# Kernel tuning notes

Measured on AMD Instinct MI355X. Metric: run time of the kernel, lower is better.

Reference implementation:

```python
import jax, jax.numpy as jnp
import numpy as np

# ---- fixed architecture hyperparameters (match init_kwargs) ----
B, S = 4, 1024
L, H, DM, DF = 4, 8, 512, 2048
DH = DM // H          # 64 head dim (= 2*R after gated SPE filter)
NS = 5                # num_sines
R = 32                # num_realizations
M = 2 * DH            # favor_feature_dims = 128 (split as +/- of 64 projections)
LN_EPS = 1e-5
ATT_EPS = 1e-6


def layernorm(x, g, b):
    mu = x.mean(-1, keepdims=True)
    var = ((x - mu) ** 2).mean(-1, keepdims=True)
    return (x - mu) * jax.lax.rsqrt(var + LN_EPS) * g + b


def sine_spe(freqs, offsets, gains, noise, seq_len):
    """SineSPE positional code. freqs/offsets/gains: (H,DH,NS); noise: (H,DH,2NS,R).
    Returns qbar, kbar of shape (S,H,DH,R)."""
    pos = jnp.arange(seq_len, dtype=freqs.dtype)
    f = jax.nn.sigmoid(freqs)[:, :, None, :] / 2.0                       # (H,DH,1,NS)
    ph_q = 2.0 * jnp.pi * f * pos[None, None, :, None] + offsets[:, :, None, :]
    ph_k = 2.0 * jnp.pi * f * pos[None, None, :, None]
    om_q = jnp.stack([jnp.cos(ph_q), jnp.sin(ph_q)], -1).reshape(H, DH, seq_len, 2 * NS)
    om_k = jnp.stack([jnp.cos(ph_k), jnp.sin(ph_k)], -1).reshape(H, DH, seq_len, 2 * NS)
    g = jax.nn.softplus(gains)
    g = jnp.stack([g, g], -1).reshape(H, DH, 2 * NS)                      # upsample gains
    z = noise * g[..., None] / jnp.sqrt(jnp.asarray(2.0 * NS, freqs.dtype))
    qbar = jnp.einsum('hdsk,hdkr->shdr', om_q, z)
    kbar = jnp.einsum('hdsk,hdkr->shdr', om_k, z)
    scale = (R * DH) ** 0.25
    return qbar / scale, kbar / scale


def spe_filter(q, k, qbar, kbar, gate, gnoise):
    """Gated SPE filter. q,k: (B,S,H,DH); qbar/kbar: (S,H,DH,R); gate: (H,DH); gnoise: (H,DH,R).
    Returns qhat, khat of shape (B,S,H,2R)."""
    g = jax.nn.sigmoid(gate)[..., None]                                   # (H,DH,1)
    gn = gnoise / (DH * R) ** 0.25
    seq_len = qbar.shape[0]
    bias = jnp.broadcast_to(jnp.sqrt(g) * gn, (seq_len, H, DH, R))
    qb = jnp.concatenate([jnp.sqrt(1.0 - g) * qbar, bias], -1)            # (S,H,DH,2R)
    kb = jnp.concatenate([jnp.sqrt(1.0 - g) * kbar, bias], -1)
    qhat = jnp.einsum('bshd,shdr->bshr', q, qb)
    khat = jnp.einsum('bshd,shdr->bshr', k, kb)
    return qhat, khat


def favor(x, omega):
    """FAVOR+ softmax feature map. x: (B,S,H,DH); omega: (DH, M//2) -> (B,S,H,M)."""
    x = x * (DH ** -0.25)                                                 # sqrt(softmax_temp), temp=1/sqrt(DH)
    half_norm = 0.5 * jnp.sum(x * x, -1, keepdims=True)
    u = jnp.einsum('bshe,em->bshm', x, omega)
    phi = jnp.concatenate([jnp.exp(u - half_norm), jnp.exp(-u - half_norm)], -1)
    return phi / jnp.sqrt(jnp.asarray(M, x.dtype))


def causal_linear_attention(Q, K, V):
    """Causal linear (kernelized) attention via lax.scan. Q,K: (B,S,H,M); V: (B,S,H,DH)."""
    Bv = Q.shape[0]

    def step(carry, qkv):
        Skv, sk = carry
        q, k, v = qkv                                                     # (B,H,M),(B,H,M),(B,H,DH)
        Skv = Skv + jnp.einsum('bhm,bhd->bhmd', k, v)
        sk = sk + k
        num = jnp.einsum('bhm,bhmd->bhd', q, Skv)
        den = jnp.einsum('bhm,bhm->bh', q, sk) + ATT_EPS
        return (Skv, sk), num / den[..., None]

    init = (jnp.zeros((Bv, H, M, DH), Q.dtype), jnp.zeros((Bv, H, M), Q.dtype))
    xs = tuple(jnp.moveaxis(t, 1, 0) for t in (Q, K, V))
    _, out = jax.lax.scan(step, init, xs)
    return jnp.moveaxis(out, 0, 1)                                        # (B,S,H,DH)


def setup_inputs() -> dict:
    key = jax.random.key(0)
    ks = jax.random.split(key, 14)

    def rn(k, shape, scale=1.0):
        return jax.random.normal(k, shape, dtype=jnp.float32) * scale

    return {
        'x': rn(ks[0], (B, S, DM)),
        'Wq': rn(ks[1], (L, DM, DM), 0.02), 'bq': jnp.zeros((L, DM), jnp.float32),
        'Wk': rn(ks[2], (L, DM, DM), 0.02), 'bk': jnp.zeros((L, DM), jnp.float32),
        'Wv': rn(ks[3], (L, DM, DM), 0.02), 'bv': jnp.zeros((L, DM), jnp.float32),
        'Wo': rn(ks[4], (L, DM, DM), 0.02), 'bo': jnp.zeros((L, DM), jnp.float32),
        'W1': rn(ks[5], (L, DM, DF), 0.02), 'b1': jnp.zeros((L, DF), jnp.float32),
        'W2': rn(ks[6], (L, DF, DM), 0.02), 'b2': jnp.zeros((L, DM), jnp.float32),
        'ln1_g': jnp.ones((L, DM), jnp.float32), 'ln1_b': jnp.zeros((L, DM), jnp.float32),
        'ln2_g': jnp.ones((L, DM), jnp.float32), 'ln2_b': jnp.zeros((L, DM), jnp.float32),
        'spe_freqs': rn(ks[7], (L, H, DH, NS)),
        'spe_offsets': rn(ks[8], (L, H, DH, NS)),
        'spe_gains': rn(ks[9], (L, H, DH, NS)),
        'spe_noise': rn(ks[10], (L, H, DH, 2 * NS, R)),
        'gate': rn(ks[11], (L, H, DH)),
        'gate_noise': rn(ks[12], (L, H, DH, R)),
        'favor_omega': rn(ks[13], (L, DH, M // 2)),
    }


def reference(x, Wq, bq, Wk, bk, Wv, bv, Wo, bo, W1, b1, W2, b2,
              ln1_g, ln1_b, ln2_g, ln2_b,
              spe_freqs, spe_offsets, spe_gains, spe_noise, gate, gate_noise, favor_omega):
    Bv, Sv, _ = x.shape
    out = x
    for l in range(L):
        qbar, kbar = sine_spe(spe_freqs[l], spe_offsets[l], spe_gains[l], spe_noise[l], Sv)
        q = (out @ Wq[l] + bq[l]).reshape(Bv, Sv, H, DH)
        k = (out @ Wk[l] + bk[l]).reshape(Bv, Sv, H, DH)
        v = (out @ Wv[l] + bv[l]).reshape(Bv, Sv, H, DH)
        qh, kh = spe_filter(q, k, qbar, kbar, gate[l], gate_noise[l])
        Qf = favor(qh, favor_omega[l])
        Kf = favor(kh, favor_omega[l])
        att = causal_linear_attention(Qf, Kf, v).reshape(Bv, Sv, DM)
        att = att @ Wo[l] + bo[l]
        h = layernorm(out + att, ln1_g[l], ln1_b[l])
        y = jax.nn.relu(h @ W1[l] + b1[l]) @ W2[l] + b2[l]
        out = layernorm(h + y, ln2_g[l], ln2_b[l])
    return out
```

## Files before the change

### kernel.cpp

```cpp
#include <hip/hip_runtime.h>
#include <math.h>

#define BB 4
#define SS 1024
#define LL 4
#define HH 8
#define DM 512
#define DF 2048
#define DH 64
#define NS 5
#define RR 32
#define MM 128
#define NC 16
#define CHK 64
#define QKV_N 1536

#define INV_SQRT10   0.316227766016838f
#define INV_SCALE    0.148650889375340f
#define TEMP_SCALE   0.353553390593274f
#define INV_SQRT_M   0.088388347648318f
#define TWO_PI       6.283185307179586f

typedef __attribute__((ext_vector_type(8))) short bf16x8;
typedef __attribute__((ext_vector_type(4))) float f32x4;

__device__ __forceinline__ unsigned short f2bf(float f) {
  union { float f; unsigned int u; } v; v.f = f;
  unsigned int r = v.u + 0x7FFFu + ((v.u >> 16) & 1u);
  return (unsigned short)(r >> 16);
}

__device__ __forceinline__ float bf2f(unsigned short u) {
  union { unsigned int u; float f; } v; v.u = (unsigned int)u << 16;
  return v.f;
}

__device__ __forceinline__ void gld_lds16(const unsigned short* g, unsigned short* l) {
  __builtin_amdgcn_global_load_lds((const __attribute__((address_space(1))) void*)g,
                                   (__attribute__((address_space(3))) void*)l,
                                   16, 0, 0);
}

template<int RELU, int OUT_BF>
__global__ __launch_bounds__(256)
void gemm_mfma(const unsigned short* __restrict__ A, const unsigned short* __restrict__ Bt,
               const float* __restrict__ bias, float* __restrict__ Cf,
               unsigned short* __restrict__ Cbf, int M, int N, int K)
{
  __shared__ unsigned short As[128 * 32];
  __shared__ unsigned short Bs[128 * 32];
  const int tid  = threadIdx.x;
  const int w    = tid >> 6;
  const int lane = tid & 63;
  const int row0 = blockIdx.y * 128;
  const int col0 = blockIdx.x * 128;
  const int wr = (w >> 1) * 64;
  const int wc = (w & 1) * 64;
  const int c0 = w * 2, c1 = w * 2 + 1;
  const int m0 = c0 * 16 + (lane >> 2);
  const int m1 = c1 * 16 + (lane >> 2);
  const int kA = (lane & 3) * 8;

  f32x4 acc[4][4] = {};

  for (int k0 = 0; k0 < K; k0 += 32) {
    gld_lds16(&A [(size_t)(row0 + m0) * K + k0 + kA], &As[c0 * 512]);
    gld_lds16(&A [(size_t)(row0 + m1) * K + k0 + kA], &As[c1 * 512]);
    gld_lds16(&Bt[(size_t)(col0 + m0) * K + k0 + kA], &Bs[c0 * 512]);
    gld_lds16(&Bt[(size_t)(col0 + m1) * K + k0 + kA], &Bs[c1 * 512]);
    __syncthreads();
    const int rA = wr + (lane & 15);
    const int rB = wc + (lane & 15);
    const int kk = (lane >> 4) * 8;
    bf16x8 af[4], bfr[4];
#pragma unroll
    for (int i = 0; i < 4; ++i) {
      af[i]  = *reinterpret_cast<const bf16x8*>(&As[(rA + i * 16) * 32 + kk]);
      bfr[i] = *reinterpret_cast<const bf16x8*>(&Bs[(rB + i * 16) * 32 + kk]);
    }
#pragma unroll
    for (int mi = 0; mi < 4; ++mi)
#pragma unroll
      for (int ni = 0; ni < 4; ++ni)
        acc[mi][ni] = __builtin_amdgcn_mfma_f32_16x16x32_bf16(af[mi], bfr[ni], acc[mi][ni], 0, 0, 0);
    __syncthreads();
  }
  const int cr = (lane >> 4) * 4;
  const int cc = lane & 15;
#pragma unroll
  for (int mi = 0; mi < 4; ++mi) {
#pragma unroll
    for (int ni = 0; ni < 4; ++ni) {
      const int col = col0 + wc + ni * 16 + cc;
      const float bv = bias[col];
#pragma unroll
      for (int r = 0; r < 4; ++r) {
        const int row = row0 + wr + mi * 16 + cr + r;
        float v = acc[mi][ni][r] + bv;
        if (RELU) v = fmaxf(v, 0.f);
        if (OUT_BF) Cbf[(size_t)row * N + col] = f2bf(v);
        else        Cf [(size_t)row * N + col] = v;
      }
    }
  }
}

template<int RELU, int OUT_BF>
__global__ __launch_bounds__(256)
void gemm_mfma_n64(const unsigned short* __restrict__ A, const unsigned short* __restrict__ Bt,
                   const float* __restrict__ bias, float* __restrict__ Cf,
                   unsigned short* __restrict__ Cbf, int M, int N, int K)
{
  __shared__ unsigned short As[128 * 32];
  __shared__ unsigned short Bs[64 * 32];
  const int tid  = threadIdx.x;
  const int w    = tid >> 6;
  const int lane = tid & 63;
  const int row0 = blockIdx.y * 128;
  const int col0 = blockIdx.x * 64;
  const int wr = (w >> 1) * 64;
  const int wc = (w & 1) * 32;
  const int c0 = w * 2, c1 = w * 2 + 1;
  const int m0 = c0 * 16 + (lane >> 2);
  const int m1 = c1 * 16 + (lane >> 2);
  const int mb = w * 16 + (lane >> 2);
  const int kA = (lane & 3) * 8;

  f32x4 acc[4][2] = {};

  for (int k0 = 0; k0 < K; k0 += 32) {
    gld_lds16(&A [(size_t)(row0 + m0) * K + k0 + kA], &As[c0 * 512]);
    gld_lds16(&A [(size_t)(row0 + m1) * K + k0 + kA], &As[c1 * 512]);
    gld_lds16(&Bt[(size_t)(col0 + mb) * K + k0 + kA], &Bs[w * 512]);
    __syncthreads();
    const int rA = wr + (lane & 15);
    const int rB = wc + (lane & 15);
    const int kk = (lane >> 4) * 8;
    bf16x8 af[4], bfr[2];
#pragma unroll
    for (int i = 0; i < 4; ++i)
      af[i]  = *reinterpret_cast<const bf16x8*>(&As[(rA + i * 16) * 32 + kk]);
#pragma unroll
    for (int i = 0; i < 2; ++i)
      bfr[i] = *reinterpret_cast<const bf16x8*>(&Bs[(rB + i * 16) * 32 + kk]);
#pragma unroll
    for (int mi = 0; mi < 4; ++mi)
#pragma unroll
      for (int ni = 0; ni < 2; ++ni)
        acc[mi][ni] = __builtin_amdgcn_mfma_f32_16x16x32_bf16(af[mi], bfr[ni], acc[mi][ni], 0, 0, 0);
    __syncthreads();
  }
  const int cr = (lane >> 4) * 4;
  const int cc = lane & 15;
#pragma unroll
  for (int mi = 0; mi < 4; ++mi) {
#pragma unroll
    for (int ni = 0; ni < 2; ++ni) {
      const int col = col0 + wc + ni * 16 + cc;
      const float bv = bias[col];
#pragma unroll
      for (int r = 0; r < 4; ++r) {
        const int row = row0 + wr + mi * 16 + cr + r;
        float v = acc[mi][ni][r] + bv;
        if (RELU) v = fmaxf(v, 0.f);
        if (OUT_BF) Cbf[(size_t)row * N + col] = f2bf(v);
        else        Cf [(size_t)row * N + col] = v;
      }
    }
  }
}

__global__ __launch_bounds__(256)
void transpose_bf(const float* __restrict__ W, unsigned short* __restrict__ Wt, int K, int N,
                  size_t inStride, size_t outStride)
{
  const float* Wl = W + blockIdx.z * inStride;
  unsigned short* Wtl = Wt + blockIdx.z * outStride;
  __shared__ float tile[32][33];
  const int k0 = blockIdx.y * 32, n0 = blockIdx.x * 32;
  const int tx = threadIdx.x & 31, ty = threadIdx.x >> 5;
#pragma unroll
  for (int j = 0; j < 4; ++j)
    tile[ty + 8 * j][tx] = Wl[(size_t)(k0 + ty + 8 * j) * N + n0 + tx];
  __syncthreads();
#pragma unroll
  for (int j = 0; j < 4; ++j)
    Wtl[(size_t)(n0 + ty + 8 * j) * K + k0 + tx] = f2bf(tile[tx][ty + 8 * j]);
}

__global__ __launch_bounds__(256)
void pack_bias(const float* __restrict__ bq, const float* __restrict__ bk,
               const float* __restrict__ bv, float* __restrict__ out)
{
  const int l = blockIdx.y;
  const int i = blockIdx.x * 256 + threadIdx.x;
  if (i < QKV_N)
    out[l * QKV_N + i] = (i < 512) ? bq[l * DM + i] : (i < 1024) ? bk[l * DM + i - 512]
                                                                 : bv[l * DM + i - 1024];
}

__global__ __launch_bounds__(256)
void cvt_bf16(const float* __restrict__ in, unsigned short* __restrict__ out, int n4)
{
  const int i = blockIdx.x * 256 + threadIdx.x;
  if (i < n4) {
    const float4 v = reinterpret_cast<const float4*>(in)[i];
    ushort4 o;
    o.x = f2bf(v.x); o.y = f2bf(v.y); o.z = f2bf(v.z); o.w = f2bf(v.w);
    reinterpret_cast<ushort4*>(out)[i] = o;
  }
}

__global__ __launch_bounds__(256)
void spe_prep_all(const float* __restrict__ gains, const float* __restrict__ noise,
                  const float* __restrict__ gate, const float* __restrict__ gnoise,
                  const float* __restrict__ offsets,
                  unsigned short* __restrict__ zpb, unsigned short* __restrict__ wbb,
                  float2* __restrict__ offcs)
{
  const int i = blockIdx.x * 256 + threadIdx.x;
  const int NZ = LL * HH * RR * 10 * DH;
  const int NW = LL * HH * RR * DH;
  const int NO = LL * HH * DH * NS;
  if (i < NZ) {
    const int d = i & 63;
    int j = i >> 6;
    const int k = j % 10; j /= 10;
    const int r = j & 31; j >>= 5;
    const int h = j & 7;  const int l = j >> 3;
    const int lhd = (l * HH + h) * DH + d;
    const float ga = gains[lhd * NS + (k >> 1)];
    const float sp = (ga > 20.f) ? ga : log1pf(__expf(ga));
    const float gg = 1.f / (1.f + __expf(-gate[lhd]));
    const float c1 = sqrtf(fmaxf(1.f - gg, 0.f));
    const float nz = noise[((size_t)lhd * 10 + k) * 32 + r];
    zpb[i] = f2bf(nz * sp * c1 * (INV_SQRT10 * INV_SCALE));
  } else if (i < NZ + NW) {
    int j = i - NZ;
    const int d = j & 63; j >>= 6;
    const int r = j & 31; j >>= 5;
    const int h = j & 7;  const int l = j >> 3;
    const int lhd = (l * HH + h) * DH + d;
    const float gg = 1.f / (1.f + __expf(-gate[lhd]));
    wbb[i - NZ] = f2bf(sqrtf(gg) * gnoise[(size_t)lhd * 32 + r] * INV_SCALE);
  } else if (i < NZ + NW + NO) {
    const int j = i - NZ - NW;
    float sn, cn;
    __sincosf(offsets[j], &sn, &cn);
    offcs[j] = make_float2(cn, sn);
  }
}

__global__ __launch_bounds__(256)
void spe_xhat(const float* __restrict__ freqs, const float2* __restrict__ offcs,
              const unsigned short* __restrict__ zpb, const unsigned short* __restrict__ wbb,
              const float* __restrict__ qkv,
              unsigned short* __restrict__ xhat, float* __restrict__ hn)
{
  const int s = blockIdx.x;
  const int h = blockIdx.y;
  const int t = threadIdx.x;
  const int w = t >> 6;
  const int lane = t & 63;
  __shared__ float omqT[10][64];
  __shared__ float omkT[10][64];
  __shared__ unsigned short qbT[64 * 64];
  __shared__ unsigned short kbT[64 * 64];
  __shared__ unsigned short rQ[16 * 64];
  __shared__ unsigned short rK[16 * 64];
  __shared__ float hqp[4][8];

  for (int e = t; e < DH * NS; e += 256) {
    const int d = e / NS, ns = e - d * NS;
    const float fr = 0.5f / (1.f + __expf(-freqs[(h * DH + d) * NS + ns]));
    float sn, cn;
    __sincosf(TWO_PI * fr * (float)s, &sn, &cn);
    const float2 oc = offcs[(h * DH + d) * NS + ns];
    omkT[2 * ns][d]     = cn;
    omkT[2 * ns + 1][d] = sn;
    omqT[2 * ns][d]     = cn * oc.x - sn * oc.y;
    omqT[2 * ns + 1][d] = sn * oc.x + cn * oc.y;
  }
  {
    const int b = t >> 6, d = t & 63;
    const size_t idx = ((size_t)b * SS + s) * QKV_N + h * DH + d;
    const int sd = d ^ ((b & 7) << 3);
    rQ[b * 64 + sd] = f2bf(qkv[idx] * TEMP_SCALE);
    rK[b * 64 + sd] = f2bf(qkv[idx + 512] * TEMP_SCALE);
  }
  for (int i = t; i < 768; i += 256) {
    rQ[256 + i] = 0;
    rK[256 + i] = 0;
  }
  __syncthreads();
  {
    const int r = t >> 3, dg = t & 7, d0 = dg * 8;
    float accq[8] = {}, acck[8] = {};
    const unsigned short* zr = zpb + (size_t)(h * RR + r) * 10 * 64 + d0;
#pragma unroll
    for (int k = 0; k < 10; ++k) {
      const bf16x8 zv = *reinterpret_cast<const bf16x8*>(zr + (size_t)k * 64);
      const float4 oq0 = *reinterpret_cast<const float4*>(&omqT[k][d0]);
      const float4 oq1 = *reinterpret_cast<const float4*>(&omqT[k][d0 + 4]);
      const float4 ok0 = *reinterpret_cast<const float4*>(&omkT[k][d0]);
      const float4 ok1 = *reinterpret_cast<const float4*>(&omkT[k][d0 + 4]);
      float zf[8];
#pragma unroll
      for (int j = 0; j < 8; ++j) zf[j] = bf2f((unsigned short)zv[j]);
      accq[0] += zf[0] * oq0.x; accq[1] += zf[1] * oq0.y;
      accq[2] += zf[2] * oq0.z; accq[3] += zf[3] * oq0.w;
      accq[4] += zf[4] * oq1.x; accq[5] += zf[5] * oq1.y;
      accq[6] += zf[6] * oq1.z; accq[7] += zf[7] * oq1.w;
      acck[0] += zf[0] * ok0.x; acck[1] += zf[1] * ok0.y;
      acck[2] += zf[2] * ok0.z; acck[3] += zf[3] * ok0.w;
      acck[4] += zf[4] * ok1.x; acck[5] += zf[5] * ok1.y;
      acck[6] += zf[6] * ok1.z; acck[7] += zf[7] * ok1.w;
    }
    bf16x8 qv, kv;
#pragma unroll
    for (int j = 0; j < 8; ++j) {
      qv[j] = (short)f2bf(accq[j]);
      kv[j] = (short)f2bf(acck[j]);
    }
    const int sd0 = d0 ^ ((r & 7) << 3);
    *reinterpret_cast<bf16x8*>(&qbT[r * 64 + sd0]) = qv;
    *reinterpret_cast<bf16x8*>(&kbT[r * 64 + sd0]) = kv;
    const bf16x8 wv = *reinterpret_cast<const bf16x8*>(&wbb[(size_t)(h * RR + r) * 64 + d0]);
    *reinterpret_cast<bf16x8*>(&qbT[(32 + r) * 64 + sd0]) = wv;
    *reinterpret_cast<bf16x8*>(&kbT[(32 + r) * 64 + sd0]) = wv;
  }
  __syncthreads();
  f32x4 aq = {0.f, 0.f, 0.f, 0.f}, ak = {0.f, 0.f, 0.f, 0.f};
  const int arow = lane & 15;
  const int colr = w * 16 + (lane & 15);
#pragma unroll
  for (int kt = 0; kt < 2; ++kt) {
    const int g = kt * 4 + (lane >> 4);
    const bf16x8 fAq = *reinterpret_cast<const bf16x8*>(&rQ[arow * 64 + ((g ^ (arow & 7)) << 3)]);
    const bf16x8 fAk = *reinterpret_cast<const bf16x8*>(&rK[arow * 64 + ((g ^ (arow & 7)) << 3)]);
    const bf16x8 fBq = *reinterpret_cast<const bf16x8*>(&qbT[colr * 64 + ((g ^ (colr & 7)) << 3)]);
    const bf16x8 fBk = *reinterpret_cast<const bf16x8*>(&kbT[colr * 64 + ((g ^ (colr & 7)) << 3)]);
    aq = __builtin_amdgcn_mfma_f32_16x16x32_bf16(fAq, fBq, aq, 0, 0, 0);
    ak = __builtin_amdgcn_mfma_f32_16x16x32_bf16(fAk, fBk, ak, 0, 0, 0);
  }
  float rq[4], rk2[4];
#pragma unroll
  for (int r = 0; r < 4; ++r) { rq[r] = aq[r] * aq[r]; rk2[r] = ak[r] * ak[r]; }
#pragma unroll
  for (int off = 1; off < 16; off <<= 1) {
#pragma unroll
    for (int r = 0; r < 4; ++r) {
      rq[r]  += __shfl_xor(rq[r],  off, 64);
      rk2[r] += __shfl_xor(rk2[r], off, 64);
    }
  }
  if (lane == 0) {
#pragma unroll
    for (int r = 0; r < 4; ++r) { hqp[w][r] = rq[r]; hqp[w][4 + r] = rk2[r]; }
  }
  if (lane < 16) {
#pragma unroll
    for (int r = 0; r < 4; ++r) {
      const size_t rowq = ((size_t)r * SS + s) * HH + h;
      xhat[rowq * 64 + w * 16 + lane] = f2bf(aq[r]);
      xhat[(rowq + (size_t)BB * SS * HH) * 64 + w * 16 + lane] = f2bf(ak[r]);
    }
  }
  __syncthreads();
  if (t < 8) {
    const int b = t & 3;
    const int ko = (t >> 2) * 4;
    const float v = 0.5f * (hqp[0][ko + b] + hqp[1][ko + b] + hqp[2][ko + b] + hqp[3][ko + b]);
    const size_t row = ((size_t)b * SS + s) * HH + h + (size_t)(t >> 2) * BB * SS * HH;
    hn[row] = v;
  }
}

__global__ __launch_bounds__(256)
void favor_gemm(const unsigned short* __restrict__ xhat, const unsigned short* __restrict__ omgT,
                const float* __restrict__ hn, unsigned short* __restrict__ QfKfB)
{
  __shared__ unsigned short As[128 * 32];
  __shared__ unsigned short Bs[64 * 32];
  const int tid  = threadIdx.x;
  const int w    = tid >> 6;
  const int lane = tid & 63;
  const int row0 = blockIdx.x * 128;
  const int c0 = w * 2, c1 = w * 2 + 1;
  const int m0 = c0 * 16 + (lane >> 2);
  const int m1 = c1 * 16 + (lane >> 2);
  const int mb = w * 16 + (lane >> 2);
  const int kA = (lane & 3) * 8;

  f32x4 acc[2][4] = {};

  for (int k0 = 0; k0 < 64; k0 += 32) {
    gld_lds16(&xhat[(size_t)(row0 + m0) * 64 + k0 + kA], &As[c0 * 512]);
    gld_lds16(&xhat[(size_t)(row0 + m1) * 64 + k0 + kA], &As[c1 * 512]);
    gld_lds16(&omgT[(size_t)mb * 64 + k0 + kA], &Bs[w * 512]);
    __syncthreads();
    const int rA = w * 32 + (lane & 15);
    const int kk = (lane >> 4) * 8;
    bf16x8 af[2], bfr[4];
#pragma unroll
    for (int i = 0; i < 2; ++i)
      af[i]  = *reinterpret_cast<const bf16x8*>(&As[(rA + i * 16) * 32 + kk]);
#pragma unroll
    for (int i = 0; i < 4; ++i)
      bfr[i] = *reinterpret_cast<const bf16x8*>(&Bs[(i * 16 + (lane & 15)) * 32 + kk]);
#pragma unroll
    for (int mi = 0; mi < 2; ++mi)
#pragma unroll
      for (int ni = 0; ni < 4; ++ni)
        acc[mi][ni] = __builtin_amdgcn_mfma_f32_16x16x32_bf16(af[mi], bfr[ni], acc[mi][ni], 0, 0, 0);
    __syncthreads();
  }
  const int cr = (lane >> 4) * 4;
  const int cc = lane & 15;
#pragma unroll
  for (int mi = 0; mi < 2; ++mi) {
#pragma unroll
    for (int r = 0; r < 4; ++r) {
      const size_t row = row0 + w * 32 + mi * 16 + cr + r;
      const float hnv = hn[row];
#pragma unroll
      for (int ni = 0; ni < 4; ++ni) {
        const int m = ni * 16 + cc;
        const float u = acc[mi][ni][r];
        QfKfB[row * MM + m]      = f2bf(__expf( u - hnv) * INV_SQRT_M);
        QfKfB[row * MM + m + 64] = f2bf(__expf(-u - hnv) * INV_SQRT_M);
      }
    }
  }
}

__global__ __launch_bounds__(256)
void attn_chunk_sums(const unsigned short* __restrict__ KfB, const float* __restrict__ qkv,
                     float* __restrict__ Sch, float* __restrict__ kch)
{
  const int c = blockIdx.x, h = blockIdx.y, b = blockIdx.z;
  const int tid = threadIdx.x;
  const int w = tid >> 6, lane = tid & 63;
  __shared__ unsigned short KcT[128 * 64];
  __shared__ unsigned short VT[64 * 64];
  const size_t srow0 = (size_t)b * SS + c * CHK;

  for (int i = tid; i < 8192; i += 256) {
    const int m = i & 127, t = i >> 7;
    KcT[m * 64 + (t ^ ((m & 7) << 3))] = KfB[((srow0 + t) * HH + h) * MM + m];
  }
  for (int i = tid; i < 4096; i += 256) {
    const int d = i & 63, tt = i >> 6;
    VT[d * 64 + (tt ^ ((d & 7) << 3))] = f2bf(qkv[(srow0 + tt) * QKV_N + 1024 + h * DH + d]);
  }
  __syncthreads();

  const int kk = (lane >> 4) * 8;
  f32x4 acc[2][4] = {};
#pragma unroll
  for (int kc = 0; kc < 2; ++kc) {
    const int k = kc * 32 + kk;
#pragma unroll
    for (int mi = 0; mi < 2; ++mi) {
      const int mA = w * 32 + mi * 16 + (lane & 15);
      const bf16x8 a = *reinterpret_cast<const bf16x8*>(&KcT[mA * 64 + (k ^ ((mA & 7) << 3))]);
#pragma unroll
      for (int ni = 0; ni < 4; ++ni) {
        const int dB = ni * 16 + (lane & 15);
        const bf16x8 bb = *reinterpret_cast<const bf16x8*>(&VT[dB * 64 + (k ^ ((dB & 7) << 3))]);
        acc[mi][ni] = __builtin_amdgcn_mfma_f32_16x16x32_bf16(a, bb, acc[mi][ni], 0, 0, 0);
      }
    }
  }
  const size_t base = (((size_t)b * HH + h) * NC + c);
  float* So = Sch + base * (MM * DH);
  const int cr = (lane >> 4) * 4, cc = lane & 15;
#pragma unroll
  for (int mi = 0; mi < 2; ++mi)
#pragma unroll
    for (int ni = 0; ni < 4; ++ni)
#pragma unroll
      for (int r = 0; r < 4; ++r)
        So[(size_t)(w * 32 + mi * 16 + cr + r) * DH + ni * 16 + cc] = acc[mi][ni][r];
  {
    const int m = tid >> 1, half = tid & 1;
    float ks = 0.f;
#pragma unroll
    for (int j = 0; j < 32; ++j) {
      const int t2 = half * 32 + j;
      ks += bf2f(KcT[m * 64 + (t2 ^ ((m & 7) << 3))]);
    }
    ks += __shfl_xor(ks, 1, 64);
    if (half == 0) kch[base * MM + m] = ks;
  }
}

__global__ __launch_bounds__(256)
void attn_scan(float* __restrict__ Sch, float* __restrict__ kch)
{
  const int bh = blockIdx.x, part = blockIdx.y;
  const int t = threadIdx.x;
  float* base = Sch + (size_t)bh * NC * (MM * DH);
  for (int e = part * 1024 + t; e < (part + 1) * 1024; e += 256) {
    float run = 0.f;
#pragma unroll
    for (int c = 0; c < NC; ++c) {
      const float v = base[(size_t)c * (MM * DH) + e];
      base[(size_t)c * (MM * DH) + e] = run;
      run += v;
    }
  }
  if (part == 0 && t < MM) {
    float* kb2 = kch + (size_t)bh * NC * MM;
    float run = 0.f;
#pragma unroll
    for (int c = 0; c < NC; ++c) {
      const float v = kb2[c * MM + t];
      kb2[c * MM + t] = run;
      run += v;
    }
  }
}

__global__ __launch_bounds__(256)
void attn_out(const unsigned short* __restrict__ QfKfB, const float* __restrict__ qkv,
              const float* __restrict__ Sch, const float* __restrict__ kch,
              unsigned short* __restrict__ att)
{
  const int c = blockIdx.x, h = blockIdx.y, b = blockIdx.z;
  const int tid = threadIdx.x;
  const int w = tid >> 6;
  const int lane = tid & 63;
  __shared__ unsigned short Qc[64 * 128];
  __shared__ unsigned short Sb[64 * 64];
  __shared__ unsigned short KVU[12288];
  __shared__ float skp[MM];
  __shared__ float denl[64];

  unsigned short* Kc   = KVU;
  unsigned short* SpxT = KVU;
  unsigned short* VT   = KVU + 8192;

  const size_t srow0 = (size_t)b * SS + c * CHK;
  const unsigned short* Qg = QfKfB + (srow0 * HH + h) * MM;
  const unsigned short* Kg = Qg + (size_t)BB * SS * HH * MM;

  if (tid < MM) skp[tid] = kch[(((size_t)b * HH + h) * NC + c) * MM + tid];

  for (int i = tid; i < 1024; i += 256) {
    const int s2 = i >> 4, m8 = (i & 15) * 8;
    const int sw = m8 ^ ((s2 & 15) << 3);
    *reinterpret_cast<bf16x8*>(&Qc[s2 * 128 + sw]) =
        *reinterpret_cast<const bf16x8*>(&Qg[(size_t)s2 * (HH * MM) + m8]);
    *reinterpret_cast<bf16x8*>(&Kc[s2 * 128 + sw]) =
        *reinterpret_cast<const bf16x8*>(&Kg[(size_t)s2 * (HH * MM) + m8]);
  }
  for (int i = tid; i < 4096; i += 256) {
    const int d = i & 63, tt = i >> 6;
    const float v = qkv[(srow0 + tt) * QKV_N + 1024 + h * DH + d];
    VT[d * 64 + (tt ^ ((d & 7) << 3))] = f2bf(v);
  }
  __syncthreads();

  const int sA = w * 16 + (lane & 15);
  const int kk = (lane >> 4) * 8;
  f32x4 acc_s[4] = {};
#pragma unroll
  for (int kc = 0; kc < 4; ++kc) {
    const int k = kc * 32 + kk;
    const bf16x8 aq = *reinterpret_cast<const bf16x8*>(&Qc[sA * 128 + (k ^ ((sA & 15) << 3))]);
#pragma unroll
    for (int n = 0; n < 4; ++n) {
      const int tB = n * 16 + (lane & 15);
      const bf16x8 bq = *reinterpret_cast<const bf16x8*>(&Kc[tB * 128 + (k ^ ((tB & 15) << 3))]);
      acc_s[n] = __builtin_amdgcn_mfma_f32_16x16x32_bf16(aq, bq, acc_s[n], 0, 0, 0);
    }
  }
  __syncthreads();

  {
    const int g = lane >> 4;
    const int tcol = lane & 15;
    float dintra[4] = {0.f, 0.f, 0.f, 0.f};
#pragma unroll
    for (int r = 0; r < 4; ++r) {
      const int s = w * 16 + g * 4 + r;
#pragma unroll
      for (int n = 0; n < 4; ++n) {
        const int t2 = n * 16 + tcol;
        const float v = (t2 <= s) ? acc_s[n][r] : 0.f;
        dintra[r] += v;
        Sb[s * 64 + (t2 ^ ((s & 7) << 3))] = f2bf(v);
      }
    }
#pragma unroll
    for (int off = 1; off < 16; off <<= 1)
#pragma unroll
      for (int r = 0; r < 4; ++r) dintra[r] += __shfl_xor(dintra[r], off, 64);
    if (tcol == 0) {
#pragma unroll
      for (int r = 0; r < 4; ++r) denl[w * 16 + g * 4 + r] = dintra[r];
    }
  }
  {
    const float* Sp = Sch + (((size_t)b * HH + h) * NC + c) * (MM * DH);
    for (int i = tid; i < 8192; i += 256) {
      const int d = i & 63, m = i >> 6;
      SpxT[d * 128 + (m ^ ((d & 15) << 3))] = f2bf(Sp[(size_t)m * DH + d]);
    }
  }
  __syncthreads();

  f32x4 acc_o[4] = {};
#pragma unroll
  for (int kc = 0; kc < 2; ++kc) {
    const int k = kc * 32 + kk;
    const bf16x8 as = *reinterpret_cast<const bf16x8*>(&Sb[sA * 64 + (k ^ ((sA & 7) << 3))]);
#pragma unroll
    for (int n = 0; n < 4; ++n) {
      const int dB = n * 16 + (lane & 15);
      const bf16x8 bv = *reinterpret_cast<const bf16x8*>(&VT[dB * 64 + (k ^ ((dB & 7) << 3))]);
      acc_o[n] = __builtin_amdgcn_mfma_f32_16x16x32_bf16(as, bv, acc_o[n], 0, 0, 0);
    }
  }
#pragma unroll
  for (int kc = 0; kc < 4; ++kc) {
    const int k = kc * 32 + kk;
    const bf16x8 aq = *reinterpret_cast<const bf16x8*>(&Qc[sA * 128 + (k ^ ((sA & 15) << 3))]);
#pragma unroll
    for (int n = 0; n < 4; ++n) {
      const int dB = n * 16 + (lane & 15);
      const bf16x8 bs = *reinterpret_cast<const bf16x8*>(&SpxT[dB * 128 + (k ^ ((dB & 15) << 3))]);
      acc_o[n] = __builtin_amdgcn_mfma_f32_16x16x32_bf16(aq, bs, acc_o[n], 0, 0, 0);
    }
  }
  {
    const int s2 = tid >> 2, part = tid & 3;
    float p = 0.f;
#pragma unroll
    for (int j = 0; j < 32; ++j) {
      const int m = part * 32 + j;
      p += bf2f(Qc[s2 * 128 + (m ^ ((s2 & 15) << 3))]) * skp[m];
    }
    p += __shfl_xor(p, 1, 64);
    p += __shfl_xor(p, 2, 64);
    if (part == 0) denl[s2] += p + 1e-6f;
  }
  __syncthreads();

  {
    const int g = lane >> 4;
    const int dcol = lane & 15;
#pragma unroll
    for (int r = 0; r < 4; ++r) {
      const int s = w * 16 + g * 4 + r;
      const float dinv = 1.f / denl[s];
#pragma unroll
      for (int n = 0; n < 4; ++n)
        att[(srow0 + s) * DM + h * DH + n * 16 + dcol] = f2bf(acc_o[n][r] * dinv);
    }
  }
}

template<int WBF>
__global__ __launch_bounds__(256)
void add_ln(const float* __restrict__ a, const float* __restrict__ bres,
            const float* __restrict__ g, const float* __restrict__ be,
            float* __restrict__ out, unsigned short* __restrict__ outbf)
{
  const int row = blockIdx.x;
  const int t = threadIdx.x;
  const size_t base = (size_t)row * DM;
  const float x0 = a[base + t] + bres[base + t];
  const float x1 = a[base + t + 256] + bres[base + t + 256];
  __shared__ float red[8];
  float ssum = x0 + x1;
#pragma unroll
  for (int off = 32; off > 0; off >>= 1) ssum += __shfl_xor(ssum, off, 64);
  const int wid = t >> 6, lid = t & 63;
  if (lid == 0) red[wid] = ssum;
  __syncthreads();
  const float mu = (red[0] + red[1] + red[2] + red[3]) * (1.f / DM);
  const float d0 = x0 - mu, d1 = x1 - mu;
  float sv = d0 * d0 + d1 * d1;
#pragma unroll
  for (int off = 32; off > 0; off >>= 1) sv += __shfl_xor(sv, off, 64);
  if (lid == 0) red[4 + wid] = sv;
  __syncthreads();
  const float var = (red[4] + red[5] + red[6] + red[7]) * (1.f / DM);
  const float rs = rsqrtf(var + 1e-5f);
  const float o0 = d0 * rs * g[t]       + be[t];
  const float o1 = d1 * rs * g[t + 256] + be[t + 256];
  out[base + t]       = o0;
  out[base + t + 256] = o1;
  if (WBF) {
    outbf[base + t]       = f2bf(o0);
    outbf[base + t + 256] = f2bf(o1);
  }
}

extern "C" void kernel_launch(void* const* d_in, const int* in_sizes, int n_in,
                              void* d_out, int out_size, void* d_ws, size_t ws_size,
                              hipStream_t stream)
{
  const float* x      = (const float*)d_in[0];
  const float* Wq     = (const float*)d_in[1];
  const float* bq     = (const float*)d_in[2];
  const float* Wk     = (const float*)d_in[3];
  const float* bk     = (const float*)d_in[4];
  const float* Wv     = (const float*)d_in[5];
  const float* bv     = (const float*)d_in[6];
  const float* Wo     = (const float*)d_in[7];
  const float* bo     = (const float*)d_in[8];
  const float* W1     = (const float*)d_in[9];
  const float* b1     = (const float*)d_in[10];
  const float* W2     = (const float*)d_in[11];
  const float* b2     = (const float*)d_in[12];
  const float* ln1g   = (const float*)d_in[13];
  const float* ln1b   = (const float*)d_in[14];
  const float* ln2g   = (const float*)d_in[15];
  const float* ln2b   = (const float*)d_in[16];
  const float* freqs  = (const float*)d_in[17];
  const float* offs   = (const float*)d_in[18];
  const float* gains  = (const float*)d_in[19];
  const float* noise  = (const float*)d_in[20];
  const float* gate   = (const float*)d_in[21];
  const float* gnoise = (const float*)d_in[22];
  const float* omega  = (const float*)d_in[23];

  float* ws = (float*)d_ws;
  size_t o = 0;
  float* curf = ws + o; o += (size_t)BB * SS * DM;
  float* qkvf = ws + o; o += (size_t)BB * SS * QKV_N;
  float* Sch  = ws + o; o += (size_t)BB * HH * NC * MM * DH;
  float* kch  = ws + o; o += (size_t)BB * HH * NC * MM;
  float* hn   = ws + o; o += (size_t)2 * BB * SS * HH;
  float* bqkv = ws + o; o += (size_t)LL * QKV_N;
  float2* offcs = (float2*)(ws + o); o += (size_t)LL * HH * DH * NS * 2;
  unsigned short* QfKfB = (unsigned short*)(ws + o); o += (size_t)2 * BB * SS * HH * MM / 2;
  unsigned short* xhat  = (unsigned short*)(ws + o); o += (size_t)2 * BB * SS * HH * DH / 2;
  unsigned short* attb  = (unsigned short*)(ws + o); o += (size_t)BB * SS * DM / 2;
  unsigned short* h_bf  = (unsigned short*)(ws + o); o += (size_t)BB * SS * DM / 2;
  unsigned short* curbf = (unsigned short*)(ws + o); o += (size_t)BB * SS * DM / 2;
  unsigned short* Wqkvt = (unsigned short*)(ws + o); o += (size_t)LL * QKV_N * DM / 2;
  unsigned short* Wot   = (unsigned short*)(ws + o); o += (size_t)LL * DM * DM / 2;
  unsigned short* W1t   = (unsigned short*)(ws + o); o += (size_t)DF * DM / 2;
  unsigned short* W2t   = (unsigned short*)(ws + o); o += (size_t)DM * DF / 2;
  unsigned short* omgT  = (unsigned short*)(ws + o); o += (size_t)LL * 4096 / 2;
  unsigned short* zpb   = (unsigned short*)(ws + o); o += (size_t)LL * HH * RR * 10 * DH / 2;
  unsigned short* wbb   = (unsigned short*)(ws + o); o += (size_t)LL * HH * RR * DH / 2;

  float* attp = qkvf;
  float* hbuf = qkvf + (size_t)2 * 1024 * 1024;
  float* ybuf = qkvf + (size_t)4 * 1024 * 1024;
  unsigned short* midbf = QfKfB;
  unsigned short* KfB   = QfKfB + (size_t)BB * SS * HH * MM;

  const int MROWS = BB * SS;

  cvt_bf16<<<(BB * SS * DM / 4 + 255) / 256, 256, 0, stream>>>(x, curbf, BB * SS * DM / 4);
  spe_prep_all<<<2856, 256, 0, stream>>>(gains, noise, gate, gnoise, offs, zpb, wbb, offcs);
  transpose_bf<<<dim3(16, 16, 4), 256, 0, stream>>>(Wq, Wqkvt,                     DM, DM, (size_t)DM * DM, (size_t)QKV_N * DM);
  transpose_bf<<<dim3(16, 16, 4), 256, 0, stream>>>(Wk, Wqkvt + (size_t)512 * DM,  DM, DM, (size_t)DM * DM, (size_t)QKV_N * DM);
  transpose_bf<<<dim3(16, 16, 4), 256, 0, stream>>>(Wv, Wqkvt + (size_t)1024 * DM, DM, DM, (size_t)DM * DM, (size_t)QKV_N * DM);
  transpose_bf<<<dim3(16, 16, 4), 256, 0, stream>>>(Wo, Wot, DM, DM, (size_t)DM * DM, (size_t)DM * DM);
  transpose_bf<<<dim3(2, 2, 4),   256, 0, stream>>>(omega, omgT, DH, MM / 2, (size_t)DH * (MM / 2), 4096);
  pack_bias<<<dim3(6, 4), 256, 0, stream>>>(bq, bk, bv, bqkv);

  for (int l = 0; l < LL; ++l) {
    const float* in = (l == 0) ? x : curf;

    gemm_mfma_n64<0, 0><<<dim3(QKV_N / 64, MROWS / 128), 256, 0, stream>>>(
        curbf, Wqkvt + (size_t)l * QKV_N * DM, bqkv + (size_t)l * QKV_N,
        qkvf, (unsigned short*)nullptr, MROWS, QKV_N, DM);

    spe_xhat<<<dim3(SS, HH), 256, 0, stream>>>(
        freqs + (size_t)l * HH * DH * NS, offcs + (size_t)l * HH * DH * NS,
        zpb + (size_t)l * HH * RR * 10 * DH, wbb + (size_t)l * HH * RR * DH,
        qkvf, xhat, hn);
    favor_gemm<<<dim3(2 * BB * SS * HH / 128), 256, 0, stream>>>(
        xhat, omgT + (size_t)l * 4096, hn, QfKfB);

    attn_chunk_sums<<<dim3(NC, HH, BB), 256, 0, stream>>>(KfB, qkvf, Sch, kch);
    attn_scan<<<dim3(BB * HH, 8), 256, 0, stream>>>(Sch, kch);
    attn_out<<<dim3(NC, HH, BB), 256, 0, stream>>>(QfKfB, qkvf, Sch, kch, attb);

    gemm_mfma_n64<0, 0><<<dim3(DM / 64, MROWS / 128), 256, 0, stream>>>(
        attb, Wot + (size_t)l * DM * DM, bo + (size_t)l * DM,
        attp, (unsigned short*)nullptr, MROWS, DM, DM);

    add_ln<1><<<MROWS, 256, 0, stream>>>(in, attp, ln1g + (size_t)l * DM, ln1b + (size_t)l * DM, hbuf, h_bf);

    transpose_bf<<<dim3(64, 16, 1), 256, 0, stream>>>(W1 + (size_t)l * DM * DF, W1t, DM, DF, 0, 0);
    gemm_mfma<1, 1><<<dim3(DF / 128, MROWS / 128), 256, 0, stream>>>(
        h_bf, W1t, b1 + (size_t)l * DF, (float*)nullptr, midbf, MROWS, DF, DM);
    transpose_bf<<<dim3(16, 64, 1), 256, 0, stream>>>(W2 + (size_t)l * DF * DM, W2t, DF, DM, 0, 0);
    gemm_mfma_n64<0, 0><<<dim3(DM / 64, MROWS / 128), 256, 0, stream>>>(
        midbf, W2t, b2 + (size_t)l * DM, ybuf, (unsigned short*)nullptr, MROWS, DM, DF);

    if (l == LL - 1) {
      add_ln<0><<<MROWS, 256, 0, stream>>>(hbuf, ybuf, ln2g + (size_t)l * DM, ln2b + (size_t)l * DM,
                                           (float*)d_out, (unsigned short*)nullptr);
    } else {
      add_ln<1><<<MROWS, 256, 0, stream>>>(hbuf, ybuf, ln2g + (size_t)l * DM, ln2b + (size_t)l * DM,
                                           curf, curbf);
    }
  }
}
```

Baseline: 740.6 us.

## Emit QKV as bf16 and vectorize attention staging loads with transposed chunk sums

```diff
diff --git a/kernel.cpp b/kernel.cpp
--- a/kernel.cpp
+++ b/kernel.cpp
@@ -215,7 +215,7 @@
 void spe_prep_all(const float* __restrict__ gains, const float* __restrict__ noise,
                   const float* __restrict__ gate, const float* __restrict__ gnoise,
                   const float* __restrict__ offsets,
-                  unsigned short* __restrict__ zpb, unsigned short* __restrict__ wbb,
+                  float* __restrict__ zpf, unsigned short* __restrict__ wbb,
                   float2* __restrict__ offcs)
 {
   const int i = blockIdx.x * 256 + threadIdx.x;
@@ -234,7 +234,7 @@
     const float gg = 1.f / (1.f + __expf(-gate[lhd]));
     const float c1 = sqrtf(fmaxf(1.f - gg, 0.f));
     const float nz = noise[((size_t)lhd * 10 + k) * 32 + r];
-    zpb[i] = f2bf(nz * sp * c1 * (INV_SQRT10 * INV_SCALE));
+    zpf[i] = nz * sp * c1 * (INV_SQRT10 * INV_SCALE * TEMP_SCALE);
   } else if (i < NZ + NW) {
     int j = i - NZ;
     const int d = j & 63; j >>= 6;
@@ -242,7 +242,7 @@
     const int h = j & 7;  const int l = j >> 3;
     const int lhd = (l * HH + h) * DH + d;
     const float gg = 1.f / (1.f + __expf(-gate[lhd]));
-    wbb[i - NZ] = f2bf(sqrtf(gg) * gnoise[(size_t)lhd * 32 + r] * INV_SCALE);
+    wbb[i - NZ] = f2bf(sqrtf(gg) * gnoise[(size_t)lhd * 32 + r] * (INV_SCALE * TEMP_SCALE));
   } else if (i < NZ + NW + NO) {
     const int j = i - NZ - NW;
     float sn, cn;
@@ -253,8 +253,8 @@
 
 __global__ __launch_bounds__(256)
 void spe_xhat(const float* __restrict__ freqs, const float2* __restrict__ offcs,
-              const unsigned short* __restrict__ zpb, const unsigned short* __restrict__ wbb,
-              const float* __restrict__ qkv,
+              const float* __restrict__ zpf, const unsigned short* __restrict__ wbb,
+              const unsigned short* __restrict__ qkvb,
               unsigned short* __restrict__ xhat, float* __restrict__ hn)
 {
   const int s = blockIdx.x;
@@ -281,40 +281,40 @@
     omqT[2 * ns][d]     = cn * oc.x - sn * oc.y;
     omqT[2 * ns + 1][d] = sn * oc.x + cn * oc.y;
   }
+  if (t < 64) {
+    const int isK = t >> 5;
+    const int b = (t >> 3) & 3;
+    const int j = t & 7;
+    const unsigned short* src = qkvb + ((size_t)b * SS + s) * QKV_N + isK * 512 + h * DH + j * 8;
+    unsigned short* dst = (isK ? rK : rQ) + b * 64 + ((j ^ b) << 3);
+    *reinterpret_cast<bf16x8*>(dst) = *reinterpret_cast<const bf16x8*>(src);
+  } else if (t < 256) {
+    const int i = t - 64;
+    bf16x8 z = {};
+    if (i < 96) *reinterpret_cast<bf16x8*>(&rQ[256 + i * 8]) = z;
+    else        *reinterpret_cast<bf16x8*>(&rK[256 + (i - 96) * 8]) = z;
+  }
+  __syncthreads();
   {
-    const int b = t >> 6, d = t & 63;
-    const size_t idx = ((size_t)b * SS + s) * QKV_N + h * DH + d;
-    const int sd = d ^ ((b & 7) << 3);
-    rQ[b * 64 + sd] = f2bf(qkv[idx] * TEMP_SCALE);
-    rK[b * 64 + sd] = f2bf(qkv[idx + 512] * TEMP_SCALE);
-  }
-  for (int i = t; i < 768; i += 256) {
-    rQ[256 + i] = 0;
-    rK[256 + i] = 0;
-  }
-  __syncthreads();
-  {
-    const int r = t >> 3, dg = t & 7, d0 = dg * 8;
+    const int r = t >> 3, d0 = (t & 7) * 8;
     float accq[8] = {}, acck[8] = {};
-    const unsigned short* zr = zpb + (size_t)(h * RR + r) * 10 * 64 + d0;
+    const float* zr = zpf + (size_t)(h * RR + r) * 640 + d0;
 #pragma unroll
     for (int k = 0; k < 10; ++k) {
-      const bf16x8 zv = *reinterpret_cast<const bf16x8*>(zr + (size_t)k * 64);
+      const float4 z0 = *reinterpret_cast<const float4*>(zr + k * 64);
+      const float4 z1 = *reinterpret_cast<const float4*>(zr + k * 64 + 4);
       const float4 oq0 = *reinterpret_cast<const float4*>(&omqT[k][d0]);
       const float4 oq1 = *reinterpret_cast<const float4*>(&omqT[k][d0 + 4]);
       const float4 ok0 = *reinterpret_cast<const float4*>(&omkT[k][d0]);
       const float4 ok1 = *reinterpret_cast<const float4*>(&omkT[k][d0 + 4]);
-      float zf[8];
-#pragma unroll
-      for (int j = 0; j < 8; ++j) zf[j] = bf2f((unsigned short)zv[j]);
-      accq[0] += zf[0] * oq0.x; accq[1] += zf[1] * oq0.y;
-      accq[2] += zf[2] * oq0.z; accq[3] += zf[3] * oq0.w;
-      accq[4] += zf[4] * oq1.x; accq[5] += zf[5] * oq1.y;
-      accq[6] += zf[6] * oq1.z; accq[7] += zf[7] * oq1.w;
-      acck[0] += zf[0] * ok0.x; acck[1] += zf[1] * ok0.y;
-      acck[2] += zf[2] * ok0.z; acck[3] += zf[3] * ok0.w;
-      acck[4] += zf[4] * ok1.x; acck[5] += zf[5] * ok1.y;
-      acck[6] += zf[6] * ok1.z; acck[7] += zf[7] * ok1.w;
+      accq[0] += z0.x * oq0.x; accq[1] += z0.y * oq0.y;
+      accq[2] += z0.z * oq0.z; accq[3] += z0.w * oq0.w;
+      accq[4] += z1.x * oq1.x; accq[5] += z1.y * oq1.y;
+      accq[6] += z1.z * oq1.z; accq[7] += z1.w * oq1.w;
+      acck[0] += z0.x * ok0.x; acck[1] += z0.y * ok0.y;
+      acck[2] += z0.z * ok0.z; acck[3] += z0.w * ok0.w;
+      acck[4] += z1.x * ok1.x; acck[5] += z1.y * ok1.y;
+      acck[6] += z1.z * ok1.z; acck[7] += z1.w * ok1.w;
     }
     bf16x8 qv, kv;
 #pragma unroll
@@ -435,7 +435,7 @@
 }
 
 __global__ __launch_bounds__(256)
-void attn_chunk_sums(const unsigned short* __restrict__ KfB, const float* __restrict__ qkv,
+void attn_chunk_sums(const unsigned short* __restrict__ KfB, const unsigned short* __restrict__ qkvb,
                      float* __restrict__ Sch, float* __restrict__ kch)
 {
   const int c = blockIdx.x, h = blockIdx.y, b = blockIdx.z;
@@ -445,30 +445,38 @@
   __shared__ unsigned short VT[64 * 64];
   const size_t srow0 = (size_t)b * SS + c * CHK;
 
-  for (int i = tid; i < 8192; i += 256) {
-    const int m = i & 127, t = i >> 7;
-    KcT[m * 64 + (t ^ ((m & 7) << 3))] = KfB[((srow0 + t) * HH + h) * MM + m];
-  }
-  for (int i = tid; i < 4096; i += 256) {
-    const int d = i & 63, tt = i >> 6;
-    VT[d * 64 + (tt ^ ((d & 7) << 3))] = f2bf(qkv[(srow0 + tt) * QKV_N + 1024 + h * DH + d]);
+  for (int i = tid; i < 1024; i += 256) {
+    const int m = i & 127, oct = i >> 7;
+    const unsigned short* src = KfB + ((srow0 + oct * 8) * HH + h) * MM + m;
+    bf16x8 v;
+#pragma unroll
+    for (int j = 0; j < 8; ++j) v[j] = (short)src[(size_t)j * (HH * MM)];
+    *reinterpret_cast<bf16x8*>(&KcT[m * 64 + ((oct << 3) ^ ((m & 7) << 3))]) = v;
+  }
+  for (int i = tid; i < 512; i += 256) {
+    const int d = i & 63, oct = i >> 6;
+    const unsigned short* src = qkvb + (srow0 + oct * 8) * QKV_N + 1024 + h * DH + d;
+    bf16x8 v;
+#pragma unroll
+    for (int j = 0; j < 8; ++j) v[j] = (short)src[(size_t)j * QKV_N];
+    *reinterpret_cast<bf16x8*>(&VT[d * 64 + ((oct << 3) ^ ((d & 7) << 3))]) = v;
   }
   __syncthreads();
 
   const int kk = (lane >> 4) * 8;
-  f32x4 acc[2][4] = {};
+  f32x4 acc[4][2] = {};
 #pragma unroll
   for (int kc = 0; kc < 2; ++kc) {
     const int k = kc * 32 + kk;
 #pragma unroll
-    for (int mi = 0; mi < 2; ++mi) {
-      const int mA = w * 32 + mi * 16 + (lane & 15);
-      const bf16x8 a = *reinterpret_cast<const bf16x8*>(&KcT[mA * 64 + (k ^ ((mA & 7) << 3))]);
-#pragma unroll
-      for (int ni = 0; ni < 4; ++ni) {
-        const int dB = ni * 16 + (lane & 15);
-        const bf16x8 bb = *reinterpret_cast<const bf16x8*>(&VT[dB * 64 + (k ^ ((dB & 7) << 3))]);
-        acc[mi][ni] = __builtin_amdgcn_mfma_f32_16x16x32_bf16(a, bb, acc[mi][ni], 0, 0, 0);
+    for (int di = 0; di < 4; ++di) {
+      const int dA = di * 16 + (lane & 15);
+      const bf16x8 a = *reinterpret_cast<const bf16x8*>(&VT[dA * 64 + (k ^ ((dA & 7) << 3))]);
+#pragma unroll
+      for (int mi = 0; mi < 2; ++mi) {
+        const int mB = w * 32 + mi * 16 + (lane & 15);
+        const bf16x8 bb = *reinterpret_cast<const bf16x8*>(&KcT[mB * 64 + (k ^ ((mB & 7) << 3))]);
+        acc[di][mi] = __builtin_amdgcn_mfma_f32_16x16x32_bf16(a, bb, acc[di][mi], 0, 0, 0);
       }
     }
   }
@@ -476,12 +484,12 @@
   float* So = Sch + base * (MM * DH);
   const int cr = (lane >> 4) * 4, cc = lane & 15;
 #pragma unroll
-  for (int mi = 0; mi < 2; ++mi)
-#pragma unroll
-    for (int ni = 0; ni < 4; ++ni)
+  for (int di = 0; di < 4; ++di)
+#pragma unroll
+    for (int mi = 0; mi < 2; ++mi)
 #pragma unroll
       for (int r = 0; r < 4; ++r)
-        So[(size_t)(w * 32 + mi * 16 + cr + r) * DH + ni * 16 + cc] = acc[mi][ni][r];
+        So[(size_t)(di * 16 + cr + r) * MM + (w * 32 + mi * 16 + cc)] = acc[di][mi][r];
   {
     const int m = tid >> 1, half = tid & 1;
     float ks = 0.f;
@@ -523,7 +531,7 @@
 }
 
 __global__ __launch_bounds__(256)
-void attn_out(const unsigned short* __restrict__ QfKfB, const float* __restrict__ qkv,
+void attn_out(const unsigned short* __restrict__ QfKfB, const unsigned short* __restrict__ qkvb,
               const float* __restrict__ Sch, const float* __restrict__ kch,
               unsigned short* __restrict__ att)
 {
@@ -555,10 +563,13 @@
     *reinterpret_cast<bf16x8*>(&Kc[s2 * 128 + sw]) =
         *reinterpret_cast<const bf16x8*>(&Kg[(size_t)s2 * (HH * MM) + m8]);
   }
-  for (int i = tid; i < 4096; i += 256) {
-    const int d = i & 63, tt = i >> 6;
-    const float v = qkv[(srow0 + tt) * QKV_N + 1024 + h * DH + d];
-    VT[d * 64 + (tt ^ ((d & 7) << 3))] = f2bf(v);
+  for (int i = tid; i < 512; i += 256) {
+    const int d = i & 63, oct = i >> 6;
+    const unsigned short* src = qkvb + (srow0 + oct * 8) * QKV_N + 1024 + h * DH + d;
+    bf16x8 v;
+#pragma unroll
+    for (int j = 0; j < 8; ++j) v[j] = (short)src[(size_t)j * QKV_N];
+    *reinterpret_cast<bf16x8*>(&VT[d * 64 + ((oct << 3) ^ ((d & 7) << 3))]) = v;
   }
   __syncthreads();
 
@@ -604,9 +615,16 @@
   }
   {
     const float* Sp = Sch + (((size_t)b * HH + h) * NC + c) * (MM * DH);
-    for (int i = tid; i < 8192; i += 256) {
-      const int d = i & 63, m = i >> 6;
-      SpxT[d * 128 + (m ^ ((d & 15) << 3))] = f2bf(Sp[(size_t)m * DH + d]);
+    for (int i = tid; i < 1024; i += 256) {
+      const int d = i >> 4, mo = (i & 15) * 8;
+      const float4 a0 = *reinterpret_cast<const float4*>(Sp + (size_t)d * MM + mo);
+      const float4 a1 = *reinterpret_cast<const float4*>(Sp + (size_t)d * MM + mo + 4);
+      bf16x8 v;
+      v[0] = (short)f2bf(a0.x); v[1] = (short)f2bf(a0.y);
+      v[2] = (short)f2bf(a0.z); v[3] = (short)f2bf(a0.w);
+      v[4] = (short)f2bf(a1.x); v[5] = (short)f2bf(a1.y);
+      v[6] = (short)f2bf(a1.z); v[7] = (short)f2bf(a1.w);
+      *reinterpret_cast<bf16x8*>(&SpxT[d * 128 + (mo ^ ((d & 15) << 3))]) = v;
     }
   }
   __syncthreads();
@@ -731,12 +749,13 @@
   float* ws = (float*)d_ws;
   size_t o = 0;
   float* curf = ws + o; o += (size_t)BB * SS * DM;
-  float* qkvf = ws + o; o += (size_t)BB * SS * QKV_N;
+  unsigned short* qkvb = (unsigned short*)(ws + o); o += (size_t)BB * SS * QKV_N / 2;
   float* Sch  = ws + o; o += (size_t)BB * HH * NC * MM * DH;
   float* kch  = ws + o; o += (size_t)BB * HH * NC * MM;
   float* hn   = ws + o; o += (size_t)2 * BB * SS * HH;
   float* bqkv = ws + o; o += (size_t)LL * QKV_N;
   float2* offcs = (float2*)(ws + o); o += (size_t)LL * HH * DH * NS * 2;
+  float* zpf  = ws + o; o += (size_t)LL * HH * RR * 10 * DH;
   unsigned short* QfKfB = (unsigned short*)(ws + o); o += (size_t)2 * BB * SS * HH * MM / 2;
   unsigned short* xhat  = (unsigned short*)(ws + o); o += (size_t)2 * BB * SS * HH * DH / 2;
   unsigned short* attb  = (unsigned short*)(ws + o); o += (size_t)BB * SS * DM / 2;
@@ -747,19 +766,18 @@
   unsigned short* W1t   = (unsigned short*)(ws + o); o += (size_t)DF * DM / 2;
   unsigned short* W2t   = (unsigned short*)(ws + o); o += (size_t)DM * DF / 2;
   unsigned short* omgT  = (unsigned short*)(ws + o); o += (size_t)LL * 4096 / 2;
-  unsigned short* zpb   = (unsigned short*)(ws + o); o += (size_t)LL * HH * RR * 10 * DH / 2;
   unsigned short* wbb   = (unsigned short*)(ws + o); o += (size_t)LL * HH * RR * DH / 2;
 
-  float* attp = qkvf;
-  float* hbuf = qkvf + (size_t)2 * 1024 * 1024;
-  float* ybuf = qkvf + (size_t)4 * 1024 * 1024;
+  float* attp = (float*)qkvb;
+  float* hbuf = Sch;
+  float* ybuf = Sch + (size_t)2 * 1024 * 1024;
   unsigned short* midbf = QfKfB;
   unsigned short* KfB   = QfKfB + (size_t)BB * SS * HH * MM;
 
   const int MROWS = BB * SS;
 
   cvt_bf16<<<(BB * SS * DM / 4 + 255) / 256, 256, 0, stream>>>(x, curbf, BB * SS * DM / 4);
-  spe_prep_all<<<2856, 256, 0, stream>>>(gains, noise, gate, gnoise, offs, zpb, wbb, offcs);
+  spe_prep_all<<<2856, 256, 0, stream>>>(gains, noise, gate, gnoise, offs, zpf, wbb, offcs);
   transpose_bf<<<dim3(16, 16, 4), 256, 0, stream>>>(Wq, Wqkvt,                     DM, DM, (size_t)DM * DM, (size_t)QKV_N * DM);
   transpose_bf<<<dim3(16, 16, 4), 256, 0, stream>>>(Wk, Wqkvt + (size_t)512 * DM,  DM, DM, (size_t)DM * DM, (size_t)QKV_N * DM);
   transpose_bf<<<dim3(16, 16, 4), 256, 0, stream>>>(Wv, Wqkvt + (size_t)1024 * DM, DM, DM, (size_t)DM * DM, (size_t)QKV_N * DM);
@@ -770,20 +788,20 @@
   for (int l = 0; l < LL; ++l) {
     const float* in = (l == 0) ? x : curf;
 
-    gemm_mfma_n64<0, 0><<<dim3(QKV_N / 64, MROWS / 128), 256, 0, stream>>>(
+    gemm_mfma_n64<0, 1><<<dim3(QKV_N / 64, MROWS / 128), 256, 0, stream>>>(
         curbf, Wqkvt + (size_t)l * QKV_N * DM, bqkv + (size_t)l * QKV_N,
-        qkvf, (unsigned short*)nullptr, MROWS, QKV_N, DM);
+        (float*)nullptr, qkvb, MROWS, QKV_N, DM);
 
     spe_xhat<<<dim3(SS, HH), 256, 0, stream>>>(
         freqs + (size_t)l * HH * DH * NS, offcs + (size_t)l * HH * DH * NS,
-        zpb + (size_t)l * HH * RR * 10 * DH, wbb + (size_t)l * HH * RR * DH,
-        qkvf, xhat, hn);
+        zpf + (size_t)l * HH * RR * 10 * DH, wbb + (size_t)l * HH * RR * DH,
+        qkvb, xhat, hn);
     favor_gemm<<<dim3(2 * BB * SS * HH / 128), 256, 0, stream>>>(
         xhat, omgT + (size_t)l * 4096, hn, QfKfB);
 
-    attn_chunk_sums<<<dim3(NC, HH, BB), 256, 0, stream>>>(KfB, qkvf, Sch, kch);
+    attn_chunk_sums<<<dim3(NC, HH, BB), 256, 0, stream>>>(KfB, qkvb, Sch, kch);
     attn_scan<<<dim3(BB * HH, 8), 256, 0, stream>>>(Sch, kch);
-    attn_out<<<dim3(NC, HH, BB), 256, 0, stream>>>(QfKfB, qkvf, Sch, kch, attb);
+    attn_out<<<dim3(NC, HH, BB), 256, 0, stream>>>(QfKfB, qkvb, Sch, kch, attb);
 
     gemm_mfma_n64<0, 0><<<dim3(DM / 64, MROWS / 128), 256, 0, stream>>>(
         attb, Wot + (size_t)l * DM * DM, bo + (size_t)l * DM,
```

Result: no change. 747.9 us (+1.0%).
